# Optimization experiments

Hardware: AMD Instinct MI355X
Metric: run time of the kernel (lower is better)

## Reference

```python
import jax, jax.numpy as jnp
import numpy as np

EPS = 1e-5

def prelu(x, a):
    return jnp.where(x >= 0, x, a * x)

def batch_norm(x, axes):
    # training-mode BatchNorm with gamma=1, beta=0 (init values)
    m = jnp.mean(x, axis=axes, keepdims=True)
    v = jnp.var(x, axis=axes, keepdims=True)
    return (x - m) / jnp.sqrt(v + EPS)

def conv_branch(X, w, b):
    # X: [B,N,F]; Conv2d(1,1,(1,k)) over the feature axis, VALID
    lhs = X[:, None, :, :]                      # [B,1,N,F]
    rhs = w.reshape(1, 1, 1, -1)                # OIHW
    out = jax.lax.conv_general_dilated(lhs, rhs, (1, 1), 'VALID',
        dimension_numbers=('NCHW', 'OIHW', 'NCHW'))
    return out[:, 0] + b                        # [B,N,F-k+1]

def setup_inputs() -> dict:
    key = jax.random.key(0)
    ks = jax.random.split(key, 16)
    B, N, F, H, D = 8192, 29, 147, 4, 128
    d_cat = 429
    s = 0.05
    return {
        'X': jax.random.normal(ks[0], (B, N, F), jnp.float32),
        'corr': jax.random.uniform(ks[1], (B, N, N), jnp.float32),
        'w_c1': s * jax.random.normal(ks[2], (3,), jnp.float32),
        'b_c1': jnp.zeros((1,), jnp.float32),
        'w_c2': s * jax.random.normal(ks[3], (5,), jnp.float32),
        'b_c2': jnp.zeros((1,), jnp.float32),
        'w_c3': s * jax.random.normal(ks[4], (7,), jnp.float32),
        'b_c3': jnp.zeros((1,), jnp.float32),
        'a_cnn': 0.25 * jnp.ones((1,), jnp.float32),
        'Wg': s * jax.random.normal(ks[5], (d_cat, D), jnp.float32),
        'bg': jnp.zeros((D,), jnp.float32),
        'a_gnn': 0.25 * jnp.ones((1,), jnp.float32),
        'centroids': jax.random.normal(ks[6], (H, 1, D), jnp.float32),
        'head_w': s * jax.random.normal(ks[7], (H,), jnp.float32),
        'Wp': s * jax.random.normal(ks[8], (D, D), jnp.float32),
        'bp': jnp.zeros((D,), jnp.float32),
        'Wm1': s * jax.random.normal(ks[9], (D, D), jnp.float32),
        'bm1': jnp.zeros((D,), jnp.float32),
        'a_mlp': 0.25 * jnp.ones((1,), jnp.float32),
        'Wm2': s * jax.random.normal(ks[10], (D, 1), jnp.float32),
        'bm2': jnp.zeros((1,), jnp.float32),
    }

def reference(X, corr, w_c1, b_c1, w_c2, b_c2, w_c3, b_c3, a_cnn,
              Wg, bg, a_gnn, centroids, head_w, Wp, bp,
              Wm1, bm1, a_mlp, Wm2, bm2):
    # three conv branches + concat + PReLU + BN over node channels
    a1 = conv_branch(X, w_c1, b_c1)             # [B,29,145]
    a2 = conv_branch(X, w_c2, b_c2)             # [B,29,143]
    a3 = conv_branch(X, w_c3, b_c3)             # [B,29,141]
    x = prelu(jnp.concatenate([a1, a2, a3], axis=2), a_cnn)  # [B,29,429]
    x = batch_norm(x, (0, 2))
    # GraphConv: A x W + b
    x = jnp.einsum('bnm,bmd->bnd', corr, x) @ Wg + bg        # [B,29,128]
    x = prelu(x, a_gnn)
    x = batch_norm(x, (0, 2))
    # CoSimPool: multi-head cosine-sim attention assignment to 1 cluster
    xn = x / (jnp.linalg.norm(x, axis=-1, keepdims=True) + 1e-8)
    cn = centroids / (jnp.linalg.norm(centroids, axis=-1, keepdims=True) + 1e-8)
    sim = jnp.einsum('hmd,bnd->bhmn', cn, xn)                # [B,4,1,29]
    agg = jnp.einsum('h,bhmn->bmn', head_w, sim)             # 1x1 conv over heads
    C = jax.nn.softmax(agg, axis=-1)                         # [B,1,29]
    x = jnp.einsum('bmn,bnd->bmd', C, x) @ Wp + bp           # [B,1,128]
    x = x[:, 0]                                              # squeeze(1)
    x = batch_norm(x, (0,))
    h = prelu(x @ Wm1 + bm1, a_mlp)
    y = jax.nn.sigmoid(h @ Wm2 + bm2)                        # [B,1]
    return y
```

## Files before the change

### kernel.cpp

```cpp
#include <hip/hip_runtime.h>

#define B_    8192
#define N_    29
#define F_    147
#define DC    429
#define D_    128
#define ROWS  (B_*N_)
#define EPSBN 1e-5f

#define UTSTR   4096
#define RS_SH   3712

#define X3_OFF   16777216
#define ACC_OFF  (X3_OFF + B_*D_)
#define BN1_OFF  (ACC_OFF)
#define BN2_OFF  (ACC_OFF + 1856)
#define BN3_OFF  (ACC_OFF + 3712)
#define FIN_OFF  (ACC_OFF + 11904)
#define CSW_OFF  (FIN_OFF + 384)
#define V_OFF    (FIN_OFF + 512)
#define V1_OFF   (FIN_OFF + 640)
#define CSWP_OFF (FIN_OFF + 768)
#define IMG_OFF  (FIN_OFF + 1024)
#define WPI_OFF  (IMG_OFF + 28672)
#define WM1I_OFF (WPI_OFF + 8192)

typedef __bf16 bf16x8 __attribute__((ext_vector_type(8)));
typedef float  f32x4  __attribute__((ext_vector_type(4)));
typedef float  f32x2  __attribute__((ext_vector_type(2)));

__device__ __forceinline__ unsigned short f2bf(float f) {
  __bf16 h = (__bf16)f;
  return __builtin_bit_cast(unsigned short, h);
}
__device__ __forceinline__ float bf2f(unsigned u16) {
  return __uint_as_float(u16 << 16);
}
__device__ __forceinline__ unsigned packbf(f32x2 v) {
  return (unsigned)f2bf(v[0]) | ((unsigned)f2bf(v[1]) << 16);
}
__device__ __forceinline__ f32x2 pfma(f32x2 a, float s, f32x2 c) {
  return __builtin_elementwise_fma(a, (f32x2){s, s}, c);
}
__device__ __forceinline__ f32x2 prelu2(f32x2 v, float a) {
  f32x2 z = (f32x2){0.f, 0.f};
  return __builtin_elementwise_fma(__builtin_elementwise_min(v, z), (f32x2){a, a},
                                   __builtin_elementwise_max(v, z));
}
__device__ __forceinline__ void gload_lds4(const float* g, void* l) {
  __builtin_amdgcn_global_load_lds((const __attribute__((address_space(1))) void*)g,
                                   (__attribute__((address_space(3))) void*)l, 4, 0, 0);
}

#define TSTR 460
#define XROW 148
#define UTILS 34
#define ATSTR 136

__global__ void k0_setup(const float* __restrict__ Wg, const float* __restrict__ Wp,
                         const float* __restrict__ Wm1, const float* __restrict__ cent,
                         const float* __restrict__ hw, float* __restrict__ ws)
{
  const int tid = threadIdx.x;
  if (blockIdx.x < 16) {
    __shared__ float cs_l[8];
    const int kb = blockIdx.x * 8;
    if (tid < 8) cs_l[tid] = 0.f;
    __syncthreads();
    unsigned short* img = (unsigned short*)(ws + IMG_OFF);
    for (int i = tid; i < 8*448; i += 256) {
      int kk = i / 448, dk = i - kk*448;
      int k = kb + kk;
      int d;
      if      (dk < 145)  d = dk;
      else if (dk == 145) d = -1;
      else if (dk < 289)  d = dk - 1;
      else if (dk == 289) d = -1;
      else if (dk < 431)  d = dk - 2;
      else                d = -1;
      float v = (d >= 0) ? Wg[(size_t)d*D_ + k] : 0.f;
      img[(size_t)k*448 + dk] = f2bf(v);
      if (d >= 0) atomicAdd(&cs_l[kk], v);
    }
    __syncthreads();
    if (tid < 8) ws[CSW_OFF + kb + tid] = cs_l[tid];
  } else if (blockIdx.x == 16) {
    unsigned short* wpi = (unsigned short*)(ws + WPI_OFF);
    for (int i = tid; i < 16384; i += 256) {
      int k = i >> 7, c = i & 127;
      wpi[c*128 + k] = f2bf(Wp[k*128 + c]);
    }
    if (tid < 128) {
      float s = 0.f;
      for (int k = 0; k < 128; ++k) s += Wp[k*128 + tid];
      ws[CSWP_OFF + tid] = s;
    }
  } else if (blockIdx.x == 17) {
    unsigned short* wmi = (unsigned short*)(ws + WM1I_OFF);
    for (int i = tid; i < 16384; i += 256) {
      int k = i >> 7, c = i & 127;
      wmi[c*128 + k] = f2bf(Wm1[k*128 + c]);
    }
  } else {
    const int wv = tid >> 6, lane = tid & 63;
    if (wv == 0) {
      float vk0 = 0.f, vk1 = 0.f;
      for (int h = 0; h < 4; ++h) {
        float c0 = cent[h*D_ + lane];
        float c1 = cent[h*D_ + 64 + lane];
        float s = c0*c0 + c1*c1;
        #pragma unroll
        for (int off = 32; off >= 1; off >>= 1) s += __shfl_xor(s, off);
        float w = hw[h] / (sqrtf(s) + 1e-8f);
        vk0 = fmaf(c0, w, vk0);
        vk1 = fmaf(c1, w, vk1);
      }
      ws[V_OFF + lane]      = vk0;
      ws[V_OFF + 64 + lane] = vk1;
      float t = vk0 + vk1;
      #pragma unroll
      for (int off = 32; off >= 1; off >>= 1) t += __shfl_xor(t, off);
      if (lane == 0) ws[V1_OFF] = t;
    } else {
      for (int i = tid - 64; i < 11904; i += 192) ws[ACC_OFF + i] = 0.f;
    }
  }
}

__global__ __launch_bounds__(256, 5) void k1_conv_gemm(
    const float* __restrict__ X,
    const float* __restrict__ wc1, const float* __restrict__ bc1,
    const float* __restrict__ wc2, const float* __restrict__ bc2,
    const float* __restrict__ wc3, const float* __restrict__ bc3,
    const float* __restrict__ acnn, float* __restrict__ ws)
{
  __shared__ __align__(16) unsigned short t_s[32*TSTR];
  const int tid = threadIdx.x;
  const int b = blockIdx.x;
  const int wv = tid >> 6, lane = tid & 63;
  const int lrow = lane & 15, quad = lane >> 4;

  {
    const float* Xb = X + (size_t)b * (N_ * F_);
    unsigned* xd = (unsigned*)t_s;
    const int r0 = wv*8, r1 = (r0 + 8 < 29) ? r0 + 8 : 29;
    for (int r = r0; r < r1; ++r) {
      const float* src = Xb + r*147;
      unsigned* dst = xd + r*XROW;
      gload_lds4(src + lane, dst);
      gload_lds4(src + 64 + lane, dst + 64);
      if (lane < 19) gload_lds4(src + 128 + lane, dst + 128);
    }
    asm volatile("s_waitcnt vmcnt(0)" ::: "memory");
    __builtin_amdgcn_sched_barrier(0);
  }

  const float c10 = wc1[0], c11 = wc1[1], c12 = wc1[2], b1 = bc1[0];
  const float c20 = wc2[0], c21 = wc2[1], c22 = wc2[2], c23 = wc2[3], c24 = wc2[4], b2 = bc2[0];
  const float c30 = wc3[0], c31 = wc3[1], c32 = wc3[2], c33 = wc3[3], c34 = wc3[4],
              c35 = wc3[5], c36 = wc3[6], b3 = bc3[0];
  const float ap = acnn[0];

  const int nC = tid >> 3, qC = tid & 7;
  const bool act = (nC < 29);
  const int f0 = qC * 18;
  const int nld = act ? nC : 28;
  float xv[24];
  {
    const f32x2* xp = (const f32x2*)((const float*)t_s + nld*XROW + f0);
    #pragma unroll
    for (int j = 0; j < 12; ++j) {
      f32x2 t = xp[j];
      xv[2*j] = t[0]; xv[2*j+1] = t[1];
    }
  }
  __syncthreads();

  for (int i = tid; i < 3*448; i += 256) {
    int r = i / 448, c = i - r*448;
    t_s[(29 + r)*TSTR + c] = 0;
  }
  for (int i = tid; i < 29*19; i += 256) {
    int n = i / 19, j = i - n*19;
    int col = (j == 0) ? 145 : ((j == 1) ? 289 : (429 + j));
    t_s[n*TSTR + col] = 0;
  }

  {
    f32x2 s1v = (f32x2){0.f,0.f}, s2v = (f32x2){0.f,0.f};
    float s1t = 0.f, s2t = 0.f;
    unsigned short* tr = t_s + nC*TSTR + f0;
    if (act) {
      const int np2 = (qC < 7) ? 9 : 8;
      const int np3 = (qC < 7) ? 9 : 7;
      #pragma unroll
      for (int j = 0; j < 9; ++j) {
        const int k = 2*j;
        f32x2 xA = (f32x2){xv[k],   xv[k+1]};
        f32x2 xB = (f32x2){xv[k+1], xv[k+2]};
        f32x2 xC = (f32x2){xv[k+2], xv[k+3]};
        {
          f32x2 v1 = pfma(xA,c10, pfma(xB,c11, pfma(xC,c12, (f32x2){b1,b1})));
          v1 = prelu2(v1, ap);
          s1v += v1; s2v = __builtin_elementwise_fma(v1, v1, s2v);
          *(unsigned*)(tr + k) = packbf(v1);
        }
        if (j < np2) {
          f32x2 xD = (f32x2){xv[k+3], xv[k+4]};
          f32x2 xE = (f32x2){xv[k+4], xv[k+5]};
          f32x2 v2 = pfma(xA,c20, pfma(xB,c21, pfma(xC,c22, pfma(xD,c23, pfma(xE,c24, (f32x2){b2,b2})))));
          v2 = prelu2(v2, ap);
          s1v += v2; s2v = __builtin_elementwise_fma(v2, v2, s2v);
          *(unsigned*)(tr + 146 + k) = packbf(v2);
        }
        if (j < np3) {
          f32x2 xD = (f32x2){xv[k+3], xv[k+4]};
          f32x2 xE = (f32x2){xv[k+4], xv[k+5]};
          f32x2 xF = (f32x2){xv[k+5], xv[k+6]};
          f32x2 xG = (f32x2){xv[k+6], xv[k+7]};
          f32x2 v3 = pfma(xA,c30, pfma(xB,c31, pfma(xC,c32, pfma(xD,c33, pfma(xE,c34, pfma(xF,c35, pfma(xG,c36, (f32x2){b3,b3})))))));
          v3 = prelu2(v3, ap);
          s1v += v3; s2v = __builtin_elementwise_fma(v3, v3, s2v);
          *(unsigned*)(tr + 290 + k) = packbf(v3);
        }
      }
      if (qC == 7) {
        float u1 = fmaf(xv[18],c10, fmaf(xv[19],c11, fmaf(xv[20],c12, b1)));
        u1 = (u1 >= 0.f) ? u1 : ap*u1;
        s1t += u1; s2t = fmaf(u1, u1, s2t);
        tr[18] = f2bf(u1);
        float u2 = fmaf(xv[16],c20, fmaf(xv[17],c21, fmaf(xv[18],c22, fmaf(xv[19],c23, fmaf(xv[20],c24, b2)))));
        u2 = (u2 >= 0.f) ? u2 : ap*u2;
        s1t += u2; s2t = fmaf(u2, u2, s2t);
        tr[146 + 16] = f2bf(u2);
        float u3 = fmaf(xv[14],c30, fmaf(xv[15],c31, fmaf(xv[16],c32, fmaf(xv[17],c33, fmaf(xv[18],c34, fmaf(xv[19],c35, fmaf(xv[20],c36, b3)))))));
        u3 = (u3 >= 0.f) ? u3 : ap*u3;
        s1t += u3; s2t = fmaf(u3, u3, s2t);
        tr[290 + 14] = f2bf(u3);
      }
    }
    float s1 = s1v[0] + s1v[1] + s1t;
    float s2 = s2v[0] + s2v[1] + s2t;
    #pragma unroll
    for (int off = 4; off >= 1; off >>= 1) {
      s1 += __shfl_xor(s1, off);
      s2 += __shfl_xor(s2, off);
    }
    if (act && qC == 0) {
      float* bn1 = ws + BN1_OFF + (size_t)(blockIdx.x & 31) * 58;
      atomicAdd(&bn1[nC*2+0], s1);
      atomicAdd(&bn1[nC*2+1], s2);
    }
  }
  __syncthreads();

  const int n0 = wv * 32;
  const unsigned short* imgp = (const unsigned short*)(ws + IMG_OFF);
  const unsigned short* gB0 = imgp + (size_t)(n0 + lrow)*448 + quad*8;
  const unsigned short* gB1 = gB0 + 16*448;
  const unsigned short* tA = t_s + quad*8;

  f32x4 a00 = (f32x4){0.f,0.f,0.f,0.f}, a01 = a00, a10 = a00, a11 = a00;
  bf16x8 Br0[4], Br1[4];
  #pragma unroll
  for (int j = 0; j < 4; ++j) {
    Br0[j] = *(const bf16x8*)(gB0 + j*32);
    Br1[j] = *(const bf16x8*)(gB1 + j*32);
  }
  #pragma unroll
  for (int ks = 0; ks < 14; ++ks) {
    bf16x8 Bc0 = Br0[ks & 3], Bc1 = Br1[ks & 3];
    if (ks < 10) {
      Br0[ks & 3] = *(const bf16x8*)(gB0 + (ks+4)*32);
      Br1[ks & 3] = *(const bf16x8*)(gB1 + (ks+4)*32);
    }
    bf16x8 A0 = *(const bf16x8*)(tA + lrow*TSTR + ks*32);
    bf16x8 A1 = *(const bf16x8*)(tA + (16+lrow)*TSTR + ks*32);
    a00 = __builtin_amdgcn_mfma_f32_16x16x32_bf16(A0, Bc0, a00, 0, 0, 0);
    a01 = __builtin_amdgcn_mfma_f32_16x16x32_bf16(A0, Bc1, a01, 0, 0, 0);
    a10 = __builtin_amdgcn_mfma_f32_16x16x32_bf16(A1, Bc0, a10, 0, 0, 0);
    a11 = __builtin_amdgcn_mfma_f32_16x16x32_bf16(A1, Bc1, a11, 0, 0, 0);
  }
  __syncthreads();

  {
    unsigned* ut32 = (unsigned*)t_s;
    const int fb0 = n0 + lrow, fb1 = n0 + 16 + lrow;
    #pragma unroll
    for (int jp = 0; jp < 2; ++jp) {
      int w = quad*2 + jp;
      ut32[fb0*17 + w]     = packbf((f32x2){a00[2*jp], a00[2*jp+1]});
      ut32[fb1*17 + w]     = packbf((f32x2){a01[2*jp], a01[2*jp+1]});
      ut32[fb0*17 + 8 + w] = packbf((f32x2){a10[2*jp], a10[2*jp+1]});
      ut32[fb1*17 + 8 + w] = packbf((f32x2){a11[2*jp], a11[2*jp+1]});
    }
  }
  __syncthreads();
  {
    const unsigned* u32t = (const unsigned*)t_s;
    unsigned short* ws16 = (unsigned short*)ws;
    unsigned* Ug = (unsigned*)(ws16 + (size_t)b * UTSTR);
    #pragma unroll
    for (int it = 0; it < 8; ++it) {
      int idx = tid + it*256;
      int f = idx >> 4, pr = idx & 15;
      Ug[f*16 + pr] = u32t[f*17 + pr];
    }
  }
}

__global__ void k2_bn1f(float* __restrict__ ws)
{
  const int n = threadIdx.x;
  if (n < 29) {
    float s1 = 0.f, s2 = 0.f;
    #pragma unroll 4
    for (int s = 0; s < 32; ++s) {
      s1 += ws[BN1_OFF + s*58 + n*2 + 0];
      s2 += ws[BN1_OFF + s*58 + n*2 + 1];
    }
    const float inv = 1.f / (float)(B_ * DC);
    float mean = s1 * inv;
    float var  = s2 * inv - mean * mean;
    ws[FIN_OFF + n]      = mean;
    ws[FIN_OFF + 32 + n] = rsqrtf(var + EPSBN);
  }
}

__global__ __launch_bounds__(256) void k3_gnn(
    const float* __restrict__ corr, const float* __restrict__ bg,
    const float* __restrict__ agnn, float* __restrict__ ws)
{
  __shared__ float cwf[841];
  __shared__ unsigned short a_s[32*40];
  __shared__ float m1s[29], is1s[29], cms[32];
  __shared__ float sts0[4][32], sts1[4][32], sts2[4][32];

  const int b = blockIdx.x, tid = threadIdx.x;
  const int wv = tid >> 6, lane = tid & 63;
  const int lrow = lane & 15, quad = lane >> 4;
  unsigned short* Utb = (unsigned short*)ws + (size_t)b * UTSTR;

  const int f0 = wv * 32;
  bf16x8 B0 = *(const bf16x8*)&Utb[(f0      + lrow)*32 + quad*8];
  bf16x8 B1 = *(const bf16x8*)&Utb[(f0 + 16 + lrow)*32 + quad*8];

  if (tid < 29) {
    m1s[tid]  = ws[FIN_OFF + tid];
    is1s[tid] = ws[FIN_OFF + 32 + tid];
  }
  const float* cb = corr + (size_t)b * 841;
  for (int i = tid; i < 841; i += 256) cwf[i] = cb[i];
  __syncthreads();

  {
    float pp[4];
    #pragma unroll
    for (int it = 0; it < 4; ++it) {
      int i = tid + it*256;
      int n = i >> 5, m = i & 31;
      bool val = (n < 29 && m < 29);
      float v = val ? cwf[n*29 + m] * is1s[m] : 0.f;
      a_s[n*40 + m] = f2bf(v);
      pp[it] = val ? v * m1s[m] : 0.f;
    }
    #pragma unroll
    for (int off = 16; off >= 1; off >>= 1) {
      #pragma unroll
      for (int it = 0; it < 4; ++it) pp[it] += __shfl_xor(pp[it], off);
    }
    #pragma unroll
    for (int it = 0; it < 4; ++it) {
      int i = tid + it*256;
      if ((i & 31) == 0 && (i >> 5) < 29) cms[i >> 5] = pp[it];
    }
  }
  __syncthreads();

  bf16x8 A0 = *(const bf16x8*)&a_s[lrow*40 + quad*8];
  bf16x8 A1 = *(const bf16x8*)&a_s[(16 + lrow)*40 + quad*8];
  f32x4 acc[2][2];
  acc[0][0] = (f32x4){0.f,0.f,0.f,0.f}; acc[0][1] = (f32x4){0.f,0.f,0.f,0.f};
  acc[1][0] = (f32x4){0.f,0.f,0.f,0.f}; acc[1][1] = (f32x4){0.f,0.f,0.f,0.f};
  acc[0][0] = __builtin_amdgcn_mfma_f32_16x16x32_bf16(A0, B0, acc[0][0], 0, 0, 0);
  acc[0][1] = __builtin_amdgcn_mfma_f32_16x16x32_bf16(A0, B1, acc[0][1], 0, 0, 0);
  acc[1][0] = __builtin_amdgcn_mfma_f32_16x16x32_bf16(A1, B0, acc[1][0], 0, 0, 0);
  acc[1][1] = __builtin_amdgcn_mfma_f32_16x16x32_bf16(A1, B1, acc[1][1], 0, 0, 0);
  __syncthreads();

  const float ag = agnn[0];
  const float vA  = ws[V_OFF  + f0 + lrow],      vB  = ws[V_OFF  + f0 + 16 + lrow];
  const float csA = ws[CSW_OFF + f0 + lrow],     csB = ws[CSW_OFF + f0 + 16 + lrow];
  const float bgA = bg[f0 + lrow],               bgB = bg[f0 + 16 + lrow];

  float psy[8], psy2[8], psv[8];
  #pragma unroll
  for (int mt = 0; mt < 2; ++mt) {
    #pragma unroll
    for (int i = 0; i < 4; ++i) {
      int idx = mt*4 + i;
      int n = mt*16 + quad*4 + i;
      float y0 = acc[mt][0][i] - cms[n & 31]*csA + bgA;
      float y1 = acc[mt][1][i] - cms[n & 31]*csB + bgB;
      y0 = (y0 >= 0.f) ? y0 : ag*y0;
      y1 = (y1 >= 0.f) ? y1 : ag*y1;
      if (n < 29) {
        Utb[n*D_ + f0 + lrow]      = f2bf(y0);
        Utb[n*D_ + f0 + 16 + lrow] = f2bf(y1);
      }
      psy[idx]  = y0 + y1;
      psy2[idx] = fmaf(y0, y0, y1*y1);
      psv[idx]  = fmaf(y0, vA, y1*vB);
    }
  }
  #pragma unroll
  for (int off = 8; off >= 1; off >>= 1) {
    #pragma unroll
    for (int idx = 0; idx < 8; ++idx) {
      psy[idx]  += __shfl_xor(psy[idx],  off);
      psy2[idx] += __shfl_xor(psy2[idx], off);
      psv[idx]  += __shfl_xor(psv[idx],  off);
    }
  }
  if (lrow == 0) {
    #pragma unroll
    for (int mt = 0; mt < 2; ++mt) {
      #pragma unroll
      for (int i = 0; i < 4; ++i) {
        int idx = mt*4 + i;
        int n = mt*16 + quad*4 + i;
        if (n < 29) {
          sts0[wv][n] = psy[idx];
          sts1[wv][n] = psy2[idx];
          sts2[wv][n] = psv[idx];
        }
      }
    }
  }
  __syncthreads();
  if (tid < 29) {
    float S1 = sts0[0][tid] + sts0[1][tid] + sts0[2][tid] + sts0[3][tid];
    float S2 = sts1[0][tid] + sts1[1][tid] + sts1[2][tid] + sts1[3][tid];
    float Sv = sts2[0][tid] + sts2[1][tid] + sts2[2][tid] + sts2[3][tid];
    float* rs = (float*)(Utb + RS_SH);
    rs[tid]      = S1;
    rs[29 + tid] = S2;
    rs[58 + tid] = Sv;
    float* bn2 = ws + BN2_OFF + (size_t)(b & 31) * 58;
    atomicAdd(&bn2[tid*2+0], S1);
    atomicAdd(&bn2[tid*2+1], S2);
  }
}

__global__ __launch_bounds__(256) void k4_pool(
    const float* __restrict__ bpv, float* __restrict__ ws)
{
  __shared__ unsigned short Atile[32*ATSTR];
  __shared__ float m2s[29], is2s[29], koffs[32];
  const int tid = threadIdx.x, wv = tid >> 6, lane = tid & 63;
  const int b0 = blockIdx.x * 32;
  const unsigned short* U16 = (const unsigned short*)ws;

  if (tid < 29) {
    float s1 = 0.f, s2 = 0.f;
    #pragma unroll 4
    for (int s = 0; s < 32; ++s) {
      s1 += ws[BN2_OFF + s*58 + tid*2 + 0];
      s2 += ws[BN2_OFF + s*58 + tid*2 + 1];
    }
    const float inv = 1.f / (float)(B_ * D_);
    float mean = s1 * inv, var = s2 * inv - mean * mean;
    m2s[tid] = mean; is2s[tid] = rsqrtf(var + EPSBN);
  }
  __syncthreads();

  const float V1 = ws[V1_OFF];
  unsigned* At32 = (unsigned*)Atile;
  for (int mb = 0; mb < 8; ++mb) {
    const int m = wv*8 + mb;
    const unsigned short* yb = U16 + (size_t)(b0 + m) * UTSTR;
    const float* rs = (const float*)(yb + RS_SH);
    float agg = -1e30f, m2 = 0.f, is2 = 0.f;
    if (lane < 29) {
      float S1 = rs[lane], S2 = rs[29+lane], Sv = rs[58+lane];
      m2 = m2s[lane]; is2 = is2s[lane];
      float ss = fmaxf(S2 - 2.f*m2*S1 + 128.f*m2*m2, 0.f);
      agg = (is2*(Sv - m2*V1)) / (is2*sqrtf(ss) + 1e-8f);
    }
    float mx = agg;
    #pragma unroll
    for (int off = 32; off >= 1; off >>= 1) mx = fmaxf(mx, __shfl_xor(mx, off));
    float e = (lane < 29) ? __expf(agg - mx) : 0.f;
    float den = e, kof = e*is2*m2;
    #pragma unroll
    for (int off = 32; off >= 1; off >>= 1) { den += __shfl_xor(den, off); kof += __shfl_xor(kof, off); }
    float rden = 1.f / den;
    float c = e * is2 * rden;
    if (lane == 0) koffs[m] = kof * rden;
    const unsigned* y32 = (const unsigned*)yb;
    float p0 = 0.f, p1 = 0.f;
    #pragma unroll
    for (int n = 0; n < 29; ++n) {
      float cn = __shfl(c, n);
      unsigned u = y32[n*64 + lane];
      p0 = fmaf(cn, bf2f(u & 0xffffu), p0);
      p1 = fmaf(cn, bf2f(u >> 16), p1);
    }
    At32[m*68 + lane] = (unsigned)f2bf(p0) | ((unsigned)f2bf(p1) << 16);
  }
  __syncthreads();

  const int lrow = lane & 15, quad = lane >> 4;
  const int n0 = wv * 32;
  const unsigned short* wpi = (const unsigned short*)(ws + WPI_OFF);
  f32x4 acc[2][2];
  acc[0][0] = (f32x4){0.f,0.f,0.f,0.f}; acc[0][1] = acc[0][0];
  acc[1][0] = acc[0][0]; acc[1][1] = acc[0][0];
  #pragma unroll
  for (int ks = 0; ks < 4; ++ks) {
    bf16x8 A0 = *(const bf16x8*)&Atile[lrow*ATSTR + ks*32 + quad*8];
    bf16x8 A1 = *(const bf16x8*)&Atile[(16+lrow)*ATSTR + ks*32 + quad*8];
    bf16x8 Bq0 = *(const bf16x8*)&wpi[(size_t)(n0 + lrow)*128 + ks*32 + quad*8];
    bf16x8 Bq1 = *(const bf16x8*)&wpi[(size_t)(n0 + 16 + lrow)*128 + ks*32 + quad*8];
    acc[0][0] = __builtin_amdgcn_mfma_f32_16x16x32_bf16(A0, Bq0, acc[0][0], 0, 0, 0);
    acc[0][1] = __builtin_amdgcn_mfma_f32_16x16x32_bf16(A0, Bq1, acc[0][1], 0, 0, 0);
    acc[1][0] = __builtin_amdgcn_mfma_f32_16x16x32_bf16(A1, Bq0, acc[1][0], 0, 0, 0);
    acc[1][1] = __builtin_amdgcn_mfma_f32_16x16x32_bf16(A1, Bq1, acc[1][1], 0, 0, 0);
  }

  float* bn3 = ws + BN3_OFF + (size_t)(blockIdx.x & 31) * 256;
  #pragma unroll
  for (int nt = 0; nt < 2; ++nt) {
    int col = n0 + nt*16 + lrow;
    float cswp = ws[CSWP_OFF + col], bp = bpv[col];
    float s1c = 0.f, s2c = 0.f;
    #pragma unroll
    for (int mt = 0; mt < 2; ++mt) {
      #pragma unroll
      for (int i = 0; i < 4; ++i) {
        int m = mt*16 + quad*4 + i;
        float x3 = acc[mt][nt][i] - koffs[m]*cswp + bp;
        ws[X3_OFF + (size_t)(b0 + m)*D_ + col] = x3;
        s1c += x3; s2c = fmaf(x3, x3, s2c);
      }
    }
    s1c += __shfl_xor(s1c, 16); s1c += __shfl_xor(s1c, 32);
    s2c += __shfl_xor(s2c, 16); s2c += __shfl_xor(s2c, 32);
    if (quad == 0) {
      atomicAdd(&bn3[col*2+0], s1c);
      atomicAdd(&bn3[col*2+1], s2c);
    }
  }
}

__global__ __launch_bounds__(256) void k5_mlp(
    const float* __restrict__ bm1, const float* __restrict__ amlp,
    const float* __restrict__ Wm2, const float* __restrict__ bm2,
    float* __restrict__ ws, float* __restrict__ out)
{
  __shared__ unsigned short Atile[32*ATSTR];
  __shared__ float m3s[128], is3s[128], logit_s[32];
  const int tid = threadIdx.x, wv = tid >> 6, lane = tid & 63;
  const int b0 = blockIdx.x * 32;

  if (tid < 128) {
    float s1 = 0.f, s2 = 0.f;
    #pragma unroll 4
    for (int s = 0; s < 32; ++s) {
      s1 += ws[BN3_OFF + s*256 + tid*2 + 0];
      s2 += ws[BN3_OFF + s*256 + tid*2 + 1];
    }
    const float inv = 1.f / (float)B_;
    float mean = s1 * inv, var = s2 * inv - mean * mean;
    m3s[tid] = mean; is3s[tid] = rsqrtf(var + EPSBN);
  }
  if (tid >= 128 && tid < 160) logit_s[tid-128] = 0.f;
  __syncthreads();

  for (int it = 0; it < 16; ++it) {
    int idx = tid + it*256;
    int row = idx >> 7, col = idx & 127;
    float v = (ws[X3_OFF + (size_t)(b0+row)*D_ + col] - m3s[col]) * is3s[col];
    Atile[row*ATSTR + col] = f2bf(v);
  }
  __syncthreads();

  const int lrow = lane & 15, quad = lane >> 4;
  const int n0 = wv * 32;
  const unsigned short* wmi = (const unsigned short*)(ws + WM1I_OFF);
  f32x4 acc[2][2];
  acc[0][0] = (f32x4){0.f,0.f,0.f,0.f}; acc[0][1] = acc[0][0];
  acc[1][0] = acc[0][0]; acc[1][1] = acc[0][0];
  #pragma unroll
  for (int ks = 0; ks < 4; ++ks) {
    bf16x8 A0 = *(const bf16x8*)&Atile[lrow*ATSTR + ks*32 + quad*8];
    bf16x8 A1 = *(const bf16x8*)&Atile[(16+lrow)*ATSTR + ks*32 + quad*8];
    bf16x8 Bq0 = *(const bf16x8*)&wmi[(size_t)(n0 + lrow)*128 + ks*32 + quad*8];
    bf16x8 Bq1 = *(const bf16x8*)&wmi[(size_t)(n0 + 16 + lrow)*128 + ks*32 + quad*8];
    acc[0][0] = __builtin_amdgcn_mfma_f32_16x16x32_bf16(A0, Bq0, acc[0][0], 0, 0, 0);
    acc[0][1] = __builtin_amdgcn_mfma_f32_16x16x32_bf16(A0, Bq1, acc[0][1], 0, 0, 0);
    acc[1][0] = __builtin_amdgcn_mfma_f32_16x16x32_bf16(A1, Bq0, acc[1][0], 0, 0, 0);
    acc[1][1] = __builtin_amdgcn_mfma_f32_16x16x32_bf16(A1, Bq1, acc[1][1], 0, 0, 0);
  }

  const float am = amlp[0];
  float bmc[2], wm2c[2];
  #pragma unroll
  for (int nt = 0; nt < 2; ++nt) {
    int col = n0 + nt*16 + lrow;
    bmc[nt] = bm1[col]; wm2c[nt] = Wm2[col];
  }
  #pragma unroll
  for (int mt = 0; mt < 2; ++mt) {
    #pragma unroll
    for (int i = 0; i < 4; ++i) {
      float pm = 0.f;
      #pragma unroll
      for (int nt = 0; nt < 2; ++nt) {
        float h = acc[mt][nt][i] + bmc[nt];
        h = (h >= 0.f) ? h : am*h;
        pm = fmaf(h, wm2c[nt], pm);
      }
      #pragma unroll
      for (int off = 8; off >= 1; off >>= 1) pm += __shfl_xor(pm, off);
      if (lrow == 0) atomicAdd(&logit_s[mt*16 + quad*4 + i], pm);
    }
  }
  __syncthreads();
  if (tid < 32) {
    float logit = logit_s[tid] + bm2[0];
    out[b0 + tid] = 1.f / (1.f + expf(-logit));
  }
}

extern "C" void kernel_launch(void* const* d_in, const int* in_sizes, int n_in,
                              void* d_out, int out_size, void* d_ws, size_t ws_size,
                              hipStream_t stream)
{
  (void)in_sizes; (void)n_in; (void)out_size; (void)ws_size;
  const float* X    = (const float*)d_in[0];
  const float* corr = (const float*)d_in[1];
  const float* wc1  = (const float*)d_in[2];
  const float* bc1  = (const float*)d_in[3];
  const float* wc2  = (const float*)d_in[4];
  const float* bc2  = (const float*)d_in[5];
  const float* wc3  = (const float*)d_in[6];
  const float* bc3  = (const float*)d_in[7];
  const float* acnn = (const float*)d_in[8];
  const float* Wg   = (const float*)d_in[9];
  const float* bg   = (const float*)d_in[10];
  const float* agnn = (const float*)d_in[11];
  const float* cent = (const float*)d_in[12];
  const float* hw   = (const float*)d_in[13];
  const float* Wp   = (const float*)d_in[14];
  const float* bp   = (const float*)d_in[15];
  const float* Wm1  = (const float*)d_in[16];
  const float* bm1  = (const float*)d_in[17];
  const float* amlp = (const float*)d_in[18];
  const float* Wm2  = (const float*)d_in[19];
  const float* bm2  = (const float*)d_in[20];
  float* ws  = (float*)d_ws;
  float* out = (float*)d_out;

  k0_setup<<<19, 256, 0, stream>>>(Wg, Wp, Wm1, cent, hw, ws);
  k1_conv_gemm<<<B_, 256, 0, stream>>>(X, wc1, bc1, wc2, bc2, wc3, bc3, acnn, ws);
  k2_bn1f<<<1, 64, 0, stream>>>(ws);
  k3_gnn<<<B_, 256, 0, stream>>>(corr, bg, agnn, ws);
  k4_pool<<<B_/32, 256, 0, stream>>>(bp, ws);
  k5_mlp<<<B_/32, 256, 0, stream>>>(bm1, amlp, Wm2, bm2, ws, out);
}
```

Baseline: 453.9 us.

## Coalesce X staging, batch two samples per GNN block, shrink pool/MLP tiles

k1 now stages each sample's X tile as one contiguous flat copy with a 147 stride instead of padded per-row copies, shrinks the LDS stride, and cuts the B-operand prefetch depth from 4 to 2. k3 handles two batch samples per block and prefetches the second sample's corr matrix into registers while the first is processed, which halves the grid. k4 and k5 switch from 32 to 16 samples per block, doubling their grids for more parallelism at the cost of half the MFMA work per wave. Unaligned LDS reads of X and the shallower prefetch may cost some latency.

```diff
diff --git a/kernel.cpp b/kernel.cpp
--- a/kernel.cpp
+++ b/kernel.cpp
@@ -52,10 +52,10 @@
                                    (__attribute__((address_space(3))) void*)l, 4, 0, 0);
 }
 
-#define TSTR 460
-#define XROW 148
+#define TSTR 456
 #define UTILS 34
 #define ATSTR 136
+#define KB4 16
 
 __global__ void k0_setup(const float* __restrict__ Wg, const float* __restrict__ Wp,
                          const float* __restrict__ Wm1, const float* __restrict__ cent,
@@ -143,17 +143,17 @@
   {
     const float* Xb = X + (size_t)b * (N_ * F_);
     unsigned* xd = (unsigned*)t_s;
-    const int r0 = wv*8, r1 = (r0 + 8 < 29) ? r0 + 8 : 29;
-    for (int r = r0; r < r1; ++r) {
-      const float* src = Xb + r*147;
-      unsigned* dst = xd + r*XROW;
-      gload_lds4(src + lane, dst);
-      gload_lds4(src + 64 + lane, dst + 64);
-      if (lane < 19) gload_lds4(src + 128 + lane, dst + 128);
-    }
-    asm volatile("s_waitcnt vmcnt(0)" ::: "memory");
-    __builtin_amdgcn_sched_barrier(0);
-  }
+    #pragma unroll
+    for (int t = 0; t < 17; ++t) {
+      int c = wv + 4*t;
+      if (c < 67) {
+        int dw = c*64 + lane;
+        int src = (dw < 4263) ? dw : 4262;
+        gload_lds4(Xb + src, xd + (size_t)c*64);
+      }
+    }
+  }
+  __syncthreads();
 
   const float c10 = wc1[0], c11 = wc1[1], c12 = wc1[2], b1 = bc1[0];
   const float c20 = wc2[0], c21 = wc2[1], c22 = wc2[2], c23 = wc2[3], c24 = wc2[4], b2 = bc2[0];
@@ -167,12 +167,9 @@
   const int nld = act ? nC : 28;
   float xv[24];
   {
-    const f32x2* xp = (const f32x2*)((const float*)t_s + nld*XROW + f0);
-    #pragma unroll
-    for (int j = 0; j < 12; ++j) {
-      f32x2 t = xp[j];
-      xv[2*j] = t[0]; xv[2*j+1] = t[1];
-    }
+    const float* xrow = (const float*)t_s + nld*147 + f0;
+    #pragma unroll
+    for (int i = 0; i < 24; ++i) xv[i] = xrow[i];
   }
   __syncthreads();
 
@@ -261,18 +258,17 @@
   const unsigned short* tA = t_s + quad*8;
 
   f32x4 a00 = (f32x4){0.f,0.f,0.f,0.f}, a01 = a00, a10 = a00, a11 = a00;
-  bf16x8 Br0[4], Br1[4];
-  #pragma unroll
-  for (int j = 0; j < 4; ++j) {
-    Br0[j] = *(const bf16x8*)(gB0 + j*32);
-    Br1[j] = *(const bf16x8*)(gB1 + j*32);
-  }
+  bf16x8 Br0[2], Br1[2];
+  Br0[0] = *(const bf16x8*)(gB0);
+  Br1[0] = *(const bf16x8*)(gB1);
+  Br0[1] = *(const bf16x8*)(gB0 + 32);
+  Br1[1] = *(const bf16x8*)(gB1 + 32);
   #pragma unroll
   for (int ks = 0; ks < 14; ++ks) {
-    bf16x8 Bc0 = Br0[ks & 3], Bc1 = Br1[ks & 3];
-    if (ks < 10) {
-      Br0[ks & 3] = *(const bf16x8*)(gB0 + (ks+4)*32);
-      Br1[ks & 3] = *(const bf16x8*)(gB1 + (ks+4)*32);
+    bf16x8 Bc0 = Br0[ks & 1], Bc1 = Br1[ks & 1];
+    if (ks < 12) {
+      Br0[ks & 1] = *(const bf16x8*)(gB0 + (ks+2)*32);
+      Br1[ks & 1] = *(const bf16x8*)(gB1 + (ks+2)*32);
     }
     bf16x8 A0 = *(const bf16x8*)(tA + lrow*TSTR + ks*32);
     bf16x8 A1 = *(const bf16x8*)(tA + (16+lrow)*TSTR + ks*32);
@@ -336,129 +332,150 @@
   __shared__ float m1s[29], is1s[29], cms[32];
   __shared__ float sts0[4][32], sts1[4][32], sts2[4][32];
 
-  const int b = blockIdx.x, tid = threadIdx.x;
+  const int b0 = blockIdx.x * 2, tid = threadIdx.x;
   const int wv = tid >> 6, lane = tid & 63;
   const int lrow = lane & 15, quad = lane >> 4;
-  unsigned short* Utb = (unsigned short*)ws + (size_t)b * UTSTR;
-
   const int f0 = wv * 32;
-  bf16x8 B0 = *(const bf16x8*)&Utb[(f0      + lrow)*32 + quad*8];
-  bf16x8 B1 = *(const bf16x8*)&Utb[(f0 + 16 + lrow)*32 + quad*8];
 
   if (tid < 29) {
     m1s[tid]  = ws[FIN_OFF + tid];
     is1s[tid] = ws[FIN_OFF + 32 + tid];
   }
-  const float* cb = corr + (size_t)b * 841;
-  for (int i = tid; i < 841; i += 256) cwf[i] = cb[i];
-  __syncthreads();
-
+  const float* cb0 = corr + (size_t)b0 * 841;
+  for (int i = tid; i < 841; i += 256) cwf[i] = cb0[i];
+  float cnx[4];
   {
-    float pp[4];
-    #pragma unroll
-    for (int it = 0; it < 4; ++it) {
-      int i = tid + it*256;
-      int n = i >> 5, m = i & 31;
-      bool val = (n < 29 && m < 29);
-      float v = val ? cwf[n*29 + m] * is1s[m] : 0.f;
-      a_s[n*40 + m] = f2bf(v);
-      pp[it] = val ? v * m1s[m] : 0.f;
-    }
-    #pragma unroll
-    for (int off = 16; off >= 1; off >>= 1) {
-      #pragma unroll
-      for (int it = 0; it < 4; ++it) pp[it] += __shfl_xor(pp[it], off);
-    }
-    #pragma unroll
-    for (int it = 0; it < 4; ++it) {
-      int i = tid + it*256;
-      if ((i & 31) == 0 && (i >> 5) < 29) cms[i >> 5] = pp[it];
-    }
-  }
-  __syncthreads();
-
-  bf16x8 A0 = *(const bf16x8*)&a_s[lrow*40 + quad*8];
-  bf16x8 A1 = *(const bf16x8*)&a_s[(16 + lrow)*40 + quad*8];
-  f32x4 acc[2][2];
-  acc[0][0] = (f32x4){0.f,0.f,0.f,0.f}; acc[0][1] = (f32x4){0.f,0.f,0.f,0.f};
-  acc[1][0] = (f32x4){0.f,0.f,0.f,0.f}; acc[1][1] = (f32x4){0.f,0.f,0.f,0.f};
-  acc[0][0] = __builtin_amdgcn_mfma_f32_16x16x32_bf16(A0, B0, acc[0][0], 0, 0, 0);
-  acc[0][1] = __builtin_amdgcn_mfma_f32_16x16x32_bf16(A0, B1, acc[0][1], 0, 0, 0);
-  acc[1][0] = __builtin_amdgcn_mfma_f32_16x16x32_bf16(A1, B0, acc[1][0], 0, 0, 0);
-  acc[1][1] = __builtin_amdgcn_mfma_f32_16x16x32_bf16(A1, B1, acc[1][1], 0, 0, 0);
-  __syncthreads();
+    const float* cb1 = cb0 + 841;
+    #pragma unroll
+    for (int k = 0; k < 4; ++k) {
+      int idx = tid + k*256;
+      cnx[k] = (idx < 841) ? cb1[idx] : 0.f;
+    }
+  }
 
   const float ag = agnn[0];
   const float vA  = ws[V_OFF  + f0 + lrow],      vB  = ws[V_OFF  + f0 + 16 + lrow];
   const float csA = ws[CSW_OFF + f0 + lrow],     csB = ws[CSW_OFF + f0 + 16 + lrow];
   const float bgA = bg[f0 + lrow],               bgB = bg[f0 + 16 + lrow];
 
-  float psy[8], psy2[8], psv[8];
-  #pragma unroll
-  for (int mt = 0; mt < 2; ++mt) {
-    #pragma unroll
-    for (int i = 0; i < 4; ++i) {
-      int idx = mt*4 + i;
-      int n = mt*16 + quad*4 + i;
-      float y0 = acc[mt][0][i] - cms[n & 31]*csA + bgA;
-      float y1 = acc[mt][1][i] - cms[n & 31]*csB + bgB;
-      y0 = (y0 >= 0.f) ? y0 : ag*y0;
-      y1 = (y1 >= 0.f) ? y1 : ag*y1;
-      if (n < 29) {
-        Utb[n*D_ + f0 + lrow]      = f2bf(y0);
-        Utb[n*D_ + f0 + 16 + lrow] = f2bf(y1);
-      }
-      psy[idx]  = y0 + y1;
-      psy2[idx] = fmaf(y0, y0, y1*y1);
-      psv[idx]  = fmaf(y0, vA, y1*vB);
-    }
-  }
-  #pragma unroll
-  for (int off = 8; off >= 1; off >>= 1) {
-    #pragma unroll
-    for (int idx = 0; idx < 8; ++idx) {
-      psy[idx]  += __shfl_xor(psy[idx],  off);
-      psy2[idx] += __shfl_xor(psy2[idx], off);
-      psv[idx]  += __shfl_xor(psv[idx],  off);
-    }
-  }
-  if (lrow == 0) {
+  #pragma unroll
+  for (int it = 0; it < 2; ++it) {
+    const int b = b0 + it;
+    unsigned short* Utb = (unsigned short*)ws + (size_t)b * UTSTR;
+
+    bf16x8 B0 = *(const bf16x8*)&Utb[(f0      + lrow)*32 + quad*8];
+    bf16x8 B1 = *(const bf16x8*)&Utb[(f0 + 16 + lrow)*32 + quad*8];
+    __syncthreads();
+
+    {
+      float pp[4];
+      #pragma unroll
+      for (int it2 = 0; it2 < 4; ++it2) {
+        int i = tid + it2*256;
+        int n = i >> 5, m = i & 31;
+        bool val = (n < 29 && m < 29);
+        float v = val ? cwf[n*29 + m] * is1s[m] : 0.f;
+        a_s[n*40 + m] = f2bf(v);
+        pp[it2] = val ? v * m1s[m] : 0.f;
+      }
+      #pragma unroll
+      for (int off = 16; off >= 1; off >>= 1) {
+        #pragma unroll
+        for (int it2 = 0; it2 < 4; ++it2) pp[it2] += __shfl_xor(pp[it2], off);
+      }
+      #pragma unroll
+      for (int it2 = 0; it2 < 4; ++it2) {
+        int i = tid + it2*256;
+        if ((i & 31) == 0 && (i >> 5) < 29) cms[i >> 5] = pp[it2];
+      }
+    }
+    __syncthreads();
+
+    if (it == 0) {
+      #pragma unroll
+      for (int k = 0; k < 4; ++k) {
+        int idx = tid + k*256;
+        if (idx < 841) cwf[idx] = cnx[k];
+      }
+    }
+
+    bf16x8 A0 = *(const bf16x8*)&a_s[lrow*40 + quad*8];
+    bf16x8 A1 = *(const bf16x8*)&a_s[(16 + lrow)*40 + quad*8];
+    f32x4 acc[2][2];
+    acc[0][0] = (f32x4){0.f,0.f,0.f,0.f}; acc[0][1] = (f32x4){0.f,0.f,0.f,0.f};
+    acc[1][0] = (f32x4){0.f,0.f,0.f,0.f}; acc[1][1] = (f32x4){0.f,0.f,0.f,0.f};
+    acc[0][0] = __builtin_amdgcn_mfma_f32_16x16x32_bf16(A0, B0, acc[0][0], 0, 0, 0);
+    acc[0][1] = __builtin_amdgcn_mfma_f32_16x16x32_bf16(A0, B1, acc[0][1], 0, 0, 0);
+    acc[1][0] = __builtin_amdgcn_mfma_f32_16x16x32_bf16(A1, B0, acc[1][0], 0, 0, 0);
+    acc[1][1] = __builtin_amdgcn_mfma_f32_16x16x32_bf16(A1, B1, acc[1][1], 0, 0, 0);
+
+    float psy[8], psy2[8], psv[8];
     #pragma unroll
     for (int mt = 0; mt < 2; ++mt) {
       #pragma unroll
       for (int i = 0; i < 4; ++i) {
         int idx = mt*4 + i;
         int n = mt*16 + quad*4 + i;
+        float y0 = acc[mt][0][i] - cms[n & 31]*csA + bgA;
+        float y1 = acc[mt][1][i] - cms[n & 31]*csB + bgB;
+        y0 = (y0 >= 0.f) ? y0 : ag*y0;
+        y1 = (y1 >= 0.f) ? y1 : ag*y1;
         if (n < 29) {
-          sts0[wv][n] = psy[idx];
-          sts1[wv][n] = psy2[idx];
-          sts2[wv][n] = psv[idx];
+          Utb[n*D_ + f0 + lrow]      = f2bf(y0);
+          Utb[n*D_ + f0 + 16 + lrow] = f2bf(y1);
         }
-      }
-    }
-  }
-  __syncthreads();
-  if (tid < 29) {
-    float S1 = sts0[0][tid] + sts0[1][tid] + sts0[2][tid] + sts0[3][tid];
-    float S2 = sts1[0][tid] + sts1[1][tid] + sts1[2][tid] + sts1[3][tid];
-    float Sv = sts2[0][tid] + sts2[1][tid] + sts2[2][tid] + sts2[3][tid];
-    float* rs = (float*)(Utb + RS_SH);
-    rs[tid]      = S1;
-    rs[29 + tid] = S2;
-    rs[58 + tid] = Sv;
-    float* bn2 = ws + BN2_OFF + (size_t)(b & 31) * 58;
-    atomicAdd(&bn2[tid*2+0], S1);
-    atomicAdd(&bn2[tid*2+1], S2);
+        psy[idx]  = y0 + y1;
+        psy2[idx] = fmaf(y0, y0, y1*y1);
+        psv[idx]  = fmaf(y0, vA, y1*vB);
+      }
+    }
+    #pragma unroll
+    for (int off = 8; off >= 1; off >>= 1) {
+      #pragma unroll
+      for (int idx = 0; idx < 8; ++idx) {
+        psy[idx]  += __shfl_xor(psy[idx],  off);
+        psy2[idx] += __shfl_xor(psy2[idx], off);
+        psv[idx]  += __shfl_xor(psv[idx],  off);
+      }
+    }
+    if (lrow == 0) {
+      #pragma unroll
+      for (int mt = 0; mt < 2; ++mt) {
+        #pragma unroll
+        for (int i = 0; i < 4; ++i) {
+          int idx = mt*4 + i;
+          int n = mt*16 + quad*4 + i;
+          if (n < 29) {
+            sts0[wv][n] = psy[idx];
+            sts1[wv][n] = psy2[idx];
+            sts2[wv][n] = psv[idx];
+          }
+        }
+      }
+    }
+    __syncthreads();
+    if (tid < 29) {
+      float S1 = sts0[0][tid] + sts0[1][tid] + sts0[2][tid] + sts0[3][tid];
+      float S2 = sts1[0][tid] + sts1[1][tid] + sts1[2][tid] + sts1[3][tid];
+      float Sv = sts2[0][tid] + sts2[1][tid] + sts2[2][tid] + sts2[3][tid];
+      float* rs = (float*)(Utb + RS_SH);
+      rs[tid]      = S1;
+      rs[29 + tid] = S2;
+      rs[58 + tid] = Sv;
+      float* bn2 = ws + BN2_OFF + (size_t)(b & 31) * 58;
+      atomicAdd(&bn2[tid*2+0], S1);
+      atomicAdd(&bn2[tid*2+1], S2);
+    }
   }
 }
 
 __global__ __launch_bounds__(256) void k4_pool(
     const float* __restrict__ bpv, float* __restrict__ ws)
 {
-  __shared__ unsigned short Atile[32*ATSTR];
-  __shared__ float m2s[29], is2s[29], koffs[32];
+  __shared__ unsigned short Atile[KB4*ATSTR];
+  __shared__ float m2s[29], is2s[29], koffs[KB4];
   const int tid = threadIdx.x, wv = tid >> 6, lane = tid & 63;
-  const int b0 = blockIdx.x * 32;
+  const int b0 = blockIdx.x * KB4;
   const unsigned short* U16 = (const unsigned short*)ws;
 
   if (tid < 29) {
@@ -476,8 +493,9 @@
 
   const float V1 = ws[V1_OFF];
   unsigned* At32 = (unsigned*)Atile;
-  for (int mb = 0; mb < 8; ++mb) {
-    const int m = wv*8 + mb;
+  #pragma unroll
+  for (int mb = 0; mb < 4; ++mb) {
+    const int m = wv*4 + mb;
     const unsigned short* yb = U16 + (size_t)(b0 + m) * UTSTR;
     const float* rs = (const float*)(yb + RS_SH);
     float agg = -1e30f, m2 = 0.f, is2 = 0.f;
@@ -513,19 +531,15 @@
   const int lrow = lane & 15, quad = lane >> 4;
   const int n0 = wv * 32;
   const unsigned short* wpi = (const unsigned short*)(ws + WPI_OFF);
-  f32x4 acc[2][2];
-  acc[0][0] = (f32x4){0.f,0.f,0.f,0.f}; acc[0][1] = acc[0][0];
-  acc[1][0] = acc[0][0]; acc[1][1] = acc[0][0];
+  f32x4 acc[2];
+  acc[0] = (f32x4){0.f,0.f,0.f,0.f}; acc[1] = acc[0];
   #pragma unroll
   for (int ks = 0; ks < 4; ++ks) {
     bf16x8 A0 = *(const bf16x8*)&Atile[lrow*ATSTR + ks*32 + quad*8];
-    bf16x8 A1 = *(const bf16x8*)&Atile[(16+lrow)*ATSTR + ks*32 + quad*8];
     bf16x8 Bq0 = *(const bf16x8*)&wpi[(size_t)(n0 + lrow)*128 + ks*32 + quad*8];
     bf16x8 Bq1 = *(const bf16x8*)&wpi[(size_t)(n0 + 16 + lrow)*128 + ks*32 + quad*8];
-    acc[0][0] = __builtin_amdgcn_mfma_f32_16x16x32_bf16(A0, Bq0, acc[0][0], 0, 0, 0);
-    acc[0][1] = __builtin_amdgcn_mfma_f32_16x16x32_bf16(A0, Bq1, acc[0][1], 0, 0, 0);
-    acc[1][0] = __builtin_amdgcn_mfma_f32_16x16x32_bf16(A1, Bq0, acc[1][0], 0, 0, 0);
-    acc[1][1] = __builtin_amdgcn_mfma_f32_16x16x32_bf16(A1, Bq1, acc[1][1], 0, 0, 0);
+    acc[0] = __builtin_amdgcn_mfma_f32_16x16x32_bf16(A0, Bq0, acc[0], 0, 0, 0);
+    acc[1] = __builtin_amdgcn_mfma_f32_16x16x32_bf16(A0, Bq1, acc[1], 0, 0, 0);
   }
 
   float* bn3 = ws + BN3_OFF + (size_t)(blockIdx.x & 31) * 256;
@@ -535,14 +549,11 @@
     float cswp = ws[CSWP_OFF + col], bp = bpv[col];
     float s1c = 0.f, s2c = 0.f;
     #pragma unroll
-    for (int mt = 0; mt < 2; ++mt) {
-      #pragma unroll
-      for (int i = 0; i < 4; ++i) {
-        int m = mt*16 + quad*4 + i;
-        float x3 = acc[mt][nt][i] - koffs[m]*cswp + bp;
-        ws[X3_OFF + (size_t)(b0 + m)*D_ + col] = x3;
-        s1c += x3; s2c = fmaf(x3, x3, s2c);
-      }
+    for (int i = 0; i < 4; ++i) {
+      int m = quad*4 + i;
+      float x3 = acc[nt][i] - koffs[m]*cswp + bp;
+      ws[X3_OFF + (size_t)(b0 + m)*D_ + col] = x3;
+      s1c += x3; s2c = fmaf(x3, x3, s2c);
     }
     s1c += __shfl_xor(s1c, 16); s1c += __shfl_xor(s1c, 32);
     s2c += __shfl_xor(s2c, 16); s2c += __shfl_xor(s2c, 32);
@@ -558,10 +569,10 @@
     const float* __restrict__ Wm2, const float* __restrict__ bm2,
     float* __restrict__ ws, float* __restrict__ out)
 {
-  __shared__ unsigned short Atile[32*ATSTR];
-  __shared__ float m3s[128], is3s[128], logit_s[32];
+  __shared__ unsigned short Atile[KB4*ATSTR];
+  __shared__ float m3s[128], is3s[128], logit_s[KB4];
   const int tid = threadIdx.x, wv = tid >> 6, lane = tid & 63;
-  const int b0 = blockIdx.x * 32;
+  const int b0 = blockIdx.x * KB4;
 
   if (tid < 128) {
     float s1 = 0.f, s2 = 0.f;
@@ -574,10 +585,11 @@
     float mean = s1 * inv, var = s2 * inv - mean * mean;
     m3s[tid] = mean; is3s[tid] = rsqrtf(var + EPSBN);
   }
-  if (tid >= 128 && tid < 160) logit_s[tid-128] = 0.f;
-  __syncthreads();
-
-  for (int it = 0; it < 16; ++it) {
+  if (tid >= 128 && tid < 128 + KB4) logit_s[tid-128] = 0.f;
+  __syncthreads();
+
+  #pragma unroll
+  for (int it = 0; it < 8; ++it) {
     int idx = tid + it*256;
     int row = idx >> 7, col = idx & 127;
     float v = (ws[X3_OFF + (size_t)(b0+row)*D_ + col] - m3s[col]) * is3s[col];
@@ -588,19 +600,15 @@
   const int lrow = lane & 15, quad = lane >> 4;
   const int n0 = wv * 32;
   const unsigned short* wmi = (const unsigned short*)(ws + WM1I_OFF);
-  f32x4 acc[2][2];
-  acc[0][0] = (f32x4){0.f,0.f,0.f,0.f}; acc[0][1] = acc[0][0];
-  acc[1][0] = acc[0][0]; acc[1][1] = acc[0][0];
+  f32x4 acc[2];
+  acc[0] = (f32x4){0.f,0.f,0.f,0.f}; acc[1] = acc[0];
   #pragma unroll
   for (int ks = 0; ks < 4; ++ks) {
     bf16x8 A0 = *(const bf16x8*)&Atile[lrow*ATSTR + ks*32 + quad*8];
-    bf16x8 A1 = *(const bf16x8*)&Atile[(16+lrow)*ATSTR + ks*32 + quad*8];
     bf16x8 Bq0 = *(const bf16x8*)&wmi[(size_t)(n0 + lrow)*128 + ks*32 + quad*8];
     bf16x8 Bq1 = *(const bf16x8*)&wmi[(size_t)(n0 + 16 + lrow)*128 + ks*32 + quad*8];
-    acc[0][0] = __builtin_amdgcn_mfma_f32_16x16x32_bf16(A0, Bq0, acc[0][0], 0, 0, 0);
-    acc[0][1] = __builtin_amdgcn_mfma_f32_16x16x32_bf16(A0, Bq1, acc[0][1], 0, 0, 0);
-    acc[1][0] = __builtin_amdgcn_mfma_f32_16x16x32_bf16(A1, Bq0, acc[1][0], 0, 0, 0);
-    acc[1][1] = __builtin_amdgcn_mfma_f32_16x16x32_bf16(A1, Bq1, acc[1][1], 0, 0, 0);
+    acc[0] = __builtin_amdgcn_mfma_f32_16x16x32_bf16(A0, Bq0, acc[0], 0, 0, 0);
+    acc[1] = __builtin_amdgcn_mfma_f32_16x16x32_bf16(A0, Bq1, acc[1], 0, 0, 0);
   }
 
   const float am = amlp[0];
@@ -611,23 +619,20 @@
     bmc[nt] = bm1[col]; wm2c[nt] = Wm2[col];
   }
   #pragma unroll
-  for (int mt = 0; mt < 2; ++mt) {
-    #pragma unroll
-    for (int i = 0; i < 4; ++i) {
-      float pm = 0.f;
-      #pragma unroll
-      for (int nt = 0; nt < 2; ++nt) {
-        float h = acc[mt][nt][i] + bmc[nt];
-        h = (h >= 0.f) ? h : am*h;
-        pm = fmaf(h, wm2c[nt], pm);
-      }
-      #pragma unroll
-      for (int off = 8; off >= 1; off >>= 1) pm += __shfl_xor(pm, off);
-      if (lrow == 0) atomicAdd(&logit_s[mt*16 + quad*4 + i], pm);
-    }
-  }
-  __syncthreads();
-  if (tid < 32) {
+  for (int i = 0; i < 4; ++i) {
+    float pm = 0.f;
+    #pragma unroll
+    for (int nt = 0; nt < 2; ++nt) {
+      float h = acc[nt][i] + bmc[nt];
+      h = (h >= 0.f) ? h : am*h;
+      pm = fmaf(h, wm2c[nt], pm);
+    }
+    #pragma unroll
+    for (int off = 8; off >= 1; off >>= 1) pm += __shfl_xor(pm, off);
+    if (lrow == 0) atomicAdd(&logit_s[quad*4 + i], pm);
+  }
+  __syncthreads();
+  if (tid < KB4) {
     float logit = logit_s[tid] + bm2[0];
     out[b0 + tid] = 1.f / (1.f + expf(-logit));
   }
@@ -665,7 +670,7 @@
   k0_setup<<<19, 256, 0, stream>>>(Wg, Wp, Wm1, cent, hw, ws);
   k1_conv_gemm<<<B_, 256, 0, stream>>>(X, wc1, bc1, wc2, bc2, wc3, bc3, acnn, ws);
   k2_bn1f<<<1, 64, 0, stream>>>(ws);
-  k3_gnn<<<B_, 256, 0, stream>>>(corr, bg, agnn, ws);
-  k4_pool<<<B_/32, 256, 0, stream>>>(bp, ws);
-  k5_mlp<<<B_/32, 256, 0, stream>>>(bm1, amlp, Wm2, bm2, ws, out);
-}
+  k3_gnn<<<B_/2, 256, 0, stream>>>(corr, bg, agnn, ws);
+  k4_pool<<<B_/KB4, 256, 0, stream>>>(bp, ws);
+  k5_mlp<<<B_/KB4, 256, 0, stream>>>(bm1, amlp, Wm2, bm2, ws, out);
+}
```

Result: no change. 447.0 us (-1.5%).
